# Optimization experiments

Hardware: AMD Instinct MI355X
Metric: run time of the kernel (lower is better)

The kernel has to match this reference:

```python
import jax, jax.numpy as jnp
import numpy as np

H = 768      # hidden_size
NH = 12      # num_attention_heads
DH = H // NH # attention_head_size
FF = 3072    # intermediate_size
E = 4        # n_expert
B, S = 8, 512
EPS = 1e-12


def _layernorm(x, g, b):
    mu = jnp.mean(x, axis=-1, keepdims=True)
    var = jnp.var(x, axis=-1, keepdims=True)
    return (x - mu) * jax.lax.rsqrt(var + EPS) * g + b


def _expert_linear(x, W, b, expert_idx):
    # W: [E, in, out], b: [E, out]; gather per-sample expert weights, then batched GEMM.
    # Mathematically identical to running every expert then slicing (single_select_fwd).
    Wg = W[expert_idx]            # [B, in, out]
    bg = b[expert_idx]            # [B, out]
    return jnp.einsum('bsi,bio->bso', x, Wg) + bg[:, None, :]


def setup_inputs() -> dict:
    key = jax.random.key(0)
    ks = jax.random.split(key, 16)
    sc = 0.02
    inp = {
        'hidden_states': jax.random.normal(ks[0], (B, S, H), jnp.float32),
        'expert_idx': jax.random.randint(ks[1], (B,), 0, E, jnp.int64) if jax.config.read('jax_enable_x64') else jax.random.randint(ks[1], (B,), 0, E).astype(jnp.int32),
        'attention_mask': jnp.zeros((B, 1, 1, S), jnp.float32),
        'Wq': sc * jax.random.normal(ks[2], (E, H, H), jnp.float32),
        'bq': jnp.zeros((E, H), jnp.float32),
        'Wk': sc * jax.random.normal(ks[3], (E, H, H), jnp.float32),
        'bk': jnp.zeros((E, H), jnp.float32),
        'Wv': sc * jax.random.normal(ks[4], (E, H, H), jnp.float32),
        'bv': jnp.zeros((E, H), jnp.float32),
        'Wo': sc * jax.random.normal(ks[5], (E, H, H), jnp.float32),
        'bo': jnp.zeros((E, H), jnp.float32),
        'ln1_g': jnp.ones((H,), jnp.float32),
        'ln1_b': jnp.zeros((H,), jnp.float32),
        'Wi': sc * jax.random.normal(ks[6], (E, H, FF), jnp.float32),
        'bi': jnp.zeros((E, FF), jnp.float32),
        'Wout': sc * jax.random.normal(ks[7], (E, FF, H), jnp.float32),
        'bout': jnp.zeros((E, H), jnp.float32),
        'ln2_g': jnp.ones((H,), jnp.float32),
        'ln2_b': jnp.zeros((H,), jnp.float32),
    }
    return inp


def reference(hidden_states, expert_idx, attention_mask, Wq, bq, Wk, bk, Wv, bv,
              Wo, bo, ln1_g, ln1_b, Wi, bi, Wout, bout, ln2_g, ln2_b):
    b, s, h = hidden_states.shape
    # --- MoE self-attention (per-sample expert QKV) ---
    q = _expert_linear(hidden_states, Wq, bq, expert_idx).reshape(b, s, NH, DH).transpose(0, 2, 1, 3)
    k = _expert_linear(hidden_states, Wk, bk, expert_idx).reshape(b, s, NH, DH).transpose(0, 2, 1, 3)
    v = _expert_linear(hidden_states, Wv, bv, expert_idx).reshape(b, s, NH, DH).transpose(0, 2, 1, 3)
    scores = jnp.einsum('bhqd,bhkd->bhqk', q, k) / np.sqrt(DH).astype(np.float32)
    scores = scores + attention_mask
    probs = jax.nn.softmax(scores, axis=-1)
    ctx = jnp.einsum('bhqk,bhkd->bhqd', probs, v).transpose(0, 2, 1, 3).reshape(b, s, h)
    # --- MoE self-output: dense + residual + LN ---
    attn_out = _expert_linear(ctx, Wo, bo, expert_idx)
    x = _layernorm(attn_out + hidden_states, ln1_g, ln1_b)
    # --- MoE FFN: intermediate (GELU) + output + residual + LN ---
    hmid = jax.nn.gelu(_expert_linear(x, Wi, bi, expert_idx), approximate=False)
    ffn = _expert_linear(hmid, Wout, bout, expert_idx)
    return _layernorm(ffn + x, ln2_g, ln2_b)
```

## Files before the change

kernel.cpp:

```cpp
#include <hip/hip_runtime.h>
#include <cstdint>
#include <cstddef>

constexpr int CB  = 8;
constexpr int CS  = 512;
constexpr int CH  = 768;
constexpr int CNH = 12;
constexpr int CDH = 64;
constexpr int CFF = 3072;
constexpr int CE  = 4;
constexpr int C3H = 3 * CH;

using f32x4  = __attribute__((ext_vector_type(4))) float;
using bf16x8 = __attribute__((ext_vector_type(8))) short;

__device__ __forceinline__ short f2bf(float x) {
  union { float f; uint32_t u; } v; v.f = x;
  return (short)((v.u + 0x7fffu + ((v.u >> 16) & 1u)) >> 16);
}

__device__ __forceinline__ void gload_lds16(const void* g, void* l) {
  __builtin_amdgcn_global_load_lds((const __attribute__((address_space(1))) void*)g,
                                   (__attribute__((address_space(3))) void*)l,
                                   16, 0, 0);
}

#define VMCNT(n)  asm volatile("s_waitcnt vmcnt(" #n ")" ::: "memory")

__global__ void cvt_bf16_kernel(const float* __restrict__ in, short* __restrict__ out, int n4) {
  int i = blockIdx.x * blockDim.x + threadIdx.x;
  if (i < n4) {
    float4 v = ((const float4*)in)[i];
    short4 o;
    o.x = f2bf(v.x); o.y = f2bf(v.y); o.z = f2bf(v.z); o.w = f2bf(v.w);
    ((short4*)out)[i] = o;
  }
}

__device__ __forceinline__ bool expert_used(const int* __restrict__ eidx, int e) {
  bool u = false;
#pragma unroll
  for (int s = 0; s < CB; ++s) u |= (eidx[s] == e);
  return u;
}

__device__ __forceinline__ void tpose_body(const float* __restrict__ Wb,
                                           short* __restrict__ Wtb, int K, int N) {
  __shared__ __align__(16) short Ts[64 * 68];
  const int n0 = blockIdx.x * 64, k0 = blockIdx.y * 64;
  const int t  = threadIdx.x;
  const int tn = t & 15, tk = t >> 4;
#pragma unroll
  for (int p = 0; p < 4; ++p) {
    int k = k0 + p * 16 + tk;
    float4 v = *(const float4*)(Wb + (size_t)k * N + n0 + tn * 4);
#pragma unroll
    for (int j = 0; j < 4; ++j)
      Ts[(tn * 4 + j) * 68 + p * 16 + tk] = f2bf(((const float*)&v)[j]);
  }
  __syncthreads();
#pragma unroll
  for (int p = 0; p < 4; ++p) {
    int n = n0 + p * 16 + tk;
    uint2 o = *(const uint2*)(Ts + (p * 16 + tk) * 68 + tn * 4);
    *(uint2*)(Wtb + (size_t)n * K + k0 + tn * 4) = o;
  }
}

__global__ void tpose_cvt_kernel(const float* __restrict__ W, short* __restrict__ Wt,
                                 const int* __restrict__ eidx, int K, int N) {
  const int e = blockIdx.z;
  if (!expert_used(eidx, e)) return;
  tpose_body(W + (size_t)e * K * N, Wt + (size_t)e * K * N, K, N);
}

__global__ void tpose4_kernel(const float* __restrict__ Wq, const float* __restrict__ Wk,
                              const float* __restrict__ Wv, const float* __restrict__ Wo,
                              const int* __restrict__ eidx,
                              short* __restrict__ Wqkvt, short* __restrict__ Wot) {
  const int z = blockIdx.z, e = z >> 2, m = z & 3;
  if (!expert_used(eidx, e)) return;
  const float* W = (m == 0) ? Wq : (m == 1) ? Wk : (m == 2) ? Wv : Wo;
  const float* Wb = W + (size_t)e * CH * CH;
  short* dst = (m == 3) ? (Wot + (size_t)e * CH * CH)
                        : (Wqkvt + ((size_t)e * C3H + m * CH) * CH);
  tpose_body(Wb, dst, CH, CH);
}

__global__ void qkv_bias_kernel(const float* __restrict__ bq, const float* __restrict__ bk,
                                const float* __restrict__ bv, float* __restrict__ dst) {
  int i = blockIdx.x * 256 + threadIdx.x;
  if (i >= CE * C3H) return;
  int e = i / C3H, r = i % C3H;
  int m = r / CH, c = r % CH;
  const float* s = (m == 0) ? bq : (m == 1) ? bk : bv;
  dst[i] = s[e * CH + c];
}

template <int BM, int BN, int TPB, int K, int NTN, int KSPLIT, int ACT, bool OB16>
__global__ __launch_bounds__(TPB, (TPB == 512 ? 2 : 3))
void gemm3_kernel(const short* __restrict__ A, const short* __restrict__ Wt,
                  const float* __restrict__ bias, const int* __restrict__ eidx,
                  char* __restrict__ out,
                  size_t wtExpStride, int biasStride, int outLd, size_t outKsStride) {
  constexpr int WAVES = TPB / 64;
  constexpr int WARPS_N = BN / 64, WARPS_M = WAVES / WARPS_N;
  constexpr int WM = BM / WARPS_M, MI = WM / 16;
  constexpr int NT = K / KSPLIT / 32;
  constexpr int JC = 4096 / BM;
  constexpr int MTS = CS / BM;
  __shared__ __align__(16) short As[2][BM * 32];
  __shared__ __align__(16) short Bs[2][BN * 32];
  const int t = threadIdx.x, w = t >> 6, l = t & 63, lr = l & 15, lg = l >> 4;

  int exv[CB];
#pragma unroll
  for (int s = 0; s < CB; ++s) exv[s] = eidx[s];
  uint32_t epack = 0;
#pragma unroll
  for (int s = 0; s < CB; ++s) epack |= (uint32_t)exv[s] << (2 * s);
  int c0 = 0, c1 = 0, c2 = 0, c3 = 0;
#pragma unroll
  for (int s = 0; s < CB; ++s) {
    c0 += (exv[s] == 0); c1 += (exv[s] == 1); c2 += (exv[s] == 2); c3 += (exv[s] == 3);
  }
  int p0 = 0, p1 = c0, p2 = c0 + c1, p3 = c0 + c1 + c2;
  uint32_t sortedPack = 0;
#pragma unroll
  for (int s = 0; s < CB; ++s) {
    int e = exv[s];
    int p = (e == 0) ? p0 : (e == 1) ? p1 : (e == 2) ? p2 : p3;
    sortedPack |= (uint32_t)s << (4 * p);
    p0 += (e == 0); p1 += (e == 1); p2 += (e == 2); p3 += (e == 3);
  }
  const int chunk = (int)gridDim.x >> 3;
  const int W_ = ((int)blockIdx.x & 7) * chunk + ((int)blockIdx.x >> 3);
  const int ks = W_ / (JC * NTN);
  const int r1 = W_ - ks * (JC * NTN);
  const int j  = r1 / NTN, nt = r1 - j * NTN;
  const int sample = (int)((sortedPack >> (4 * (j / MTS))) & 7);
  const int jj = j % MTS;
  const int e  = (int)((epack >> (2 * sample)) & 3);
  const int mrow0 = sample * CS + jj * BM;
  const int kBase = ks * NT * 32;

  const int srow = t >> 2;
  const int gcol = (((t & 3) ^ ((t >> 3) & 3)) * 8);
  const short* aSrc = A + (size_t)(mrow0 + srow) * K + kBase + gcol;
  const short* bSrc = Wt + (size_t)e * wtExpStride + (size_t)(nt * BN + srow) * K + kBase + gcol;
  constexpr int ROWS_PER_ISS = TPB / 4;
  const size_t issStride = (size_t)ROWS_PER_ISS * K;

  const int wrow = (w / WARPS_N) * WM, wn = (w % WARPS_N) * 64;
  const int rswz = (lg ^ ((lr >> 1) & 3)) * 8;
  int aoff[MI], boff[4];
#pragma unroll
  for (int mi = 0; mi < MI; ++mi) aoff[mi] = (wrow + mi * 16 + lr) * 32 + rswz;
#pragma unroll
  for (int ni = 0; ni < 4; ++ni)  boff[ni] = (wn + ni * 16 + lr) * 32 + rswz;

  f32x4 acc[MI][4] = {};

  auto STAGE = [&](int buf, int kt) {
    const short* as = aSrc + kt * 32;
#pragma unroll
    for (int i = 0; i < BM / ROWS_PER_ISS; ++i)
      gload_lds16(as + i * issStride, &As[buf][i * TPB * 8 + t * 8]);
    const short* bs = bSrc + kt * 32;
#pragma unroll
    for (int i = 0; i < BN / ROWS_PER_ISS; ++i)
      gload_lds16(bs + i * issStride, &Bs[buf][i * TPB * 8 + t * 8]);
  };

  STAGE(0, 0);
  VMCNT(0);
  __builtin_amdgcn_s_barrier();
  __builtin_amdgcn_sched_barrier(0);

  for (int kt = 0; kt < NT; ++kt) {
    const int buf = kt & 1;
    if (kt + 1 < NT) STAGE(buf ^ 1, kt + 1);
    bf16x8 bfr[4], af[MI];
#pragma unroll
    for (int ni = 0; ni < 4; ++ni)  bfr[ni] = *(const bf16x8*)(&Bs[buf][boff[ni]]);
#pragma unroll
    for (int mi = 0; mi < MI; ++mi) af[mi] = *(const bf16x8*)(&As[buf][aoff[mi]]);
    __builtin_amdgcn_s_setprio(1);
#pragma unroll
    for (int mi = 0; mi < MI; ++mi)
#pragma unroll
      for (int ni = 0; ni < 4; ++ni)
        acc[mi][ni] = __builtin_amdgcn_mfma_f32_16x16x32_bf16(af[mi], bfr[ni], acc[mi][ni], 0, 0, 0);
    __builtin_amdgcn_s_setprio(0);
    VMCNT(0);
    __builtin_amdgcn_s_barrier();
    __builtin_amdgcn_sched_barrier(0);
  }

  float* outF = (float*)out + (size_t)ks * outKsStride;
#pragma unroll
  for (int ni = 0; ni < 4; ++ni) {
    const int col = nt * BN + wn + ni * 16 + lr;
    const float bv = bias ? bias[e * biasStride + col] : 0.0f;
#pragma unroll
    for (int mi = 0; mi < MI; ++mi) {
      const int row0 = mrow0 + wrow + mi * 16 + lg * 4;
#pragma unroll
      for (int r = 0; r < 4; ++r) {
        float v = acc[mi][ni][r] + bv;
        if (ACT == 1) v = 0.5f * v * (1.0f + erff(v * 0.70710678118654752f));
        if (OB16) ((short*)out)[(size_t)(row0 + r) * outLd + col] = f2bf(v);
        else      outF[(size_t)(row0 + r) * outLd + col] = v;
      }
    }
  }
}

__global__ void attn_kernel(const short* __restrict__ QKV, const float* __restrict__ mask,
                            short* __restrict__ ctx) {
  __shared__ __align__(16) short Vt[2][64 * 40];
  __shared__ __align__(16) short Pt[4][2][16 * 40];
  const int bh = blockIdx.x;
  const int b = bh / CNH, h = bh % CNH;
  const int qt = blockIdx.y;
  const int t = threadIdx.x, w = t >> 6, l = t & 63, lr = l & 15, lg = l >> 4;

  const size_t bS = (size_t)b * CS;
  const short* Qh = QKV + bS * C3H + h * CDH;
  const short* Kh = Qh + CH;
  const short* Vh = Qh + 2 * CH;
  const float* mrow = mask + bS;

  const int qrow = qt * 64 + w * 16 + lr;
  bf16x8 qa[2];
  qa[0] = *(const bf16x8*)(Qh + (size_t)qrow * C3H + lg * 8);
  qa[1] = *(const bf16x8*)(Qh + (size_t)qrow * C3H + 32 + lg * 8);

  f32x4 o[4] = {};
  float lp[4] = {0.f, 0.f, 0.f, 0.f};

  const int dh = t & 63, kg = t >> 6;
  {
    short v8[8];
#pragma unroll
    for (int j = 0; j < 8; ++j) v8[j] = Vh[(size_t)(kg * 8 + j) * C3H + dh];
    uint32_t p0 = (uint32_t)(uint16_t)v8[0] | ((uint32_t)(uint16_t)v8[1] << 16);
    uint32_t p1 = (uint32_t)(uint16_t)v8[2] | ((uint32_t)(uint16_t)v8[3] << 16);
    uint32_t p2 = (uint32_t)(uint16_t)v8[4] | ((uint32_t)(uint16_t)v8[5] << 16);
    uint32_t p3 = (uint32_t)(uint16_t)v8[6] | ((uint32_t)(uint16_t)v8[7] << 16);
    uint4 pk = {p0, p1, p2, p3};
    *(uint4*)(&Vt[0][dh * 40 + kg * 8]) = pk;
  }

  for (int tt = 0; tt < CS / 32; ++tt) {
    const int k0 = tt * 32;
    __syncthreads();

    f32x4 sacc[2] = {};
#pragma unroll
    for (int n = 0; n < 2; ++n) {
      bf16x8 kb0 = *(const bf16x8*)(Kh + (size_t)(k0 + n * 16 + lr) * C3H + lg * 8);
      bf16x8 kb1 = *(const bf16x8*)(Kh + (size_t)(k0 + n * 16 + lr) * C3H + 32 + lg * 8);
      sacc[n] = __builtin_amdgcn_mfma_f32_16x16x32_bf16(qa[0], kb0, sacc[n], 0, 0, 0);
      sacc[n] = __builtin_amdgcn_mfma_f32_16x16x32_bf16(qa[1], kb1, sacc[n], 0, 0, 0);
    }

    if (tt + 1 < CS / 32) {
      const int k1 = k0 + 32;
      short v8[8];
#pragma unroll
      for (int j = 0; j < 8; ++j) v8[j] = Vh[(size_t)(k1 + kg * 8 + j) * C3H + dh];
      uint32_t p0 = (uint32_t)(uint16_t)v8[0] | ((uint32_t)(uint16_t)v8[1] << 16);
      uint32_t p1 = (uint32_t)(uint16_t)v8[2] | ((uint32_t)(uint16_t)v8[3] << 16);
      uint32_t p2 = (uint32_t)(uint16_t)v8[4] | ((uint32_t)(uint16_t)v8[5] << 16);
      uint32_t p3 = (uint32_t)(uint16_t)v8[6] | ((uint32_t)(uint16_t)v8[7] << 16);
      uint4 pk = {p0, p1, p2, p3};
      *(uint4*)(&Vt[(tt + 1) & 1][dh * 40 + kg * 8]) = pk;
    }

    const int pb = tt & 1;
#pragma unroll
    for (int n = 0; n < 2; ++n) {
      float mv = mrow[k0 + n * 16 + lr];
#pragma unroll
      for (int r = 0; r < 4; ++r) {
        float s = sacc[n][r] * 0.125f + mv;
        float e = __expf(s);
        lp[r] += e;
        Pt[w][pb][(lg * 4 + r) * 40 + n * 16 + lr] = f2bf(e);
      }
    }

    bf16x8 pa = *(const bf16x8*)(&Pt[w][pb][lr * 40 + lg * 8]);
#pragma unroll
    for (int d = 0; d < 4; ++d) {
      bf16x8 vbf = *(const bf16x8*)(&Vt[tt & 1][(d * 16 + lr) * 40 + lg * 8]);
      o[d] = __builtin_amdgcn_mfma_f32_16x16x32_bf16(pa, vbf, o[d], 0, 0, 0);
    }
  }

#pragma unroll
  for (int r = 0; r < 4; ++r) {
    float s = lp[r];
    s += __shfl_xor(s, 1); s += __shfl_xor(s, 2);
    s += __shfl_xor(s, 4); s += __shfl_xor(s, 8);
    lp[r] = 1.0f / s;
  }
#pragma unroll
  for (int d = 0; d < 4; ++d)
#pragma unroll
    for (int r = 0; r < 4; ++r) {
      int row = qt * 64 + w * 16 + lg * 4 + r;
      ctx[(bS + row) * CH + h * CDH + d * 16 + lr] = f2bf(o[d][r] * lp[r]);
    }
}

__global__ void ln_kernel(const float* __restrict__ xin, const float* __restrict__ res,
                          const float* __restrict__ g, const float* __restrict__ bta,
                          float* __restrict__ out32, short* __restrict__ out16) {
  const int row = blockIdx.x;
  const int l = threadIdx.x;
  const float* xr = xin + (size_t)row * CH;
  const float* rr = res + (size_t)row * CH;
  float4 v[3];
  float sum = 0.f, ss = 0.f;
#pragma unroll
  for (int j = 0; j < 3; ++j) {
    float4 a = *(const float4*)(xr + j * 256 + l * 4);
    float4 b = *(const float4*)(rr + j * 256 + l * 4);
    a.x += b.x; a.y += b.y; a.z += b.z; a.w += b.w;
    v[j] = a;
    sum += a.x + a.y + a.z + a.w;
    ss  += a.x * a.x + a.y * a.y + a.z * a.z + a.w * a.w;
  }
#pragma unroll
  for (int m = 1; m < 64; m <<= 1) { sum += __shfl_xor(sum, m); ss += __shfl_xor(ss, m); }
  const float mean = sum * (1.0f / CH);
  const float var  = ss * (1.0f / CH) - mean * mean;
  const float rstd = rsqrtf(var + 1e-12f);
#pragma unroll
  for (int j = 0; j < 3; ++j) {
    float4 gg = *(const float4*)(g   + j * 256 + l * 4);
    float4 bb = *(const float4*)(bta + j * 256 + l * 4);
    float4 a = v[j], y;
    y.x = (a.x - mean) * rstd * gg.x + bb.x;
    y.y = (a.y - mean) * rstd * gg.y + bb.y;
    y.z = (a.z - mean) * rstd * gg.z + bb.z;
    y.w = (a.w - mean) * rstd * gg.w + bb.w;
    *(float4*)(out32 + (size_t)row * CH + j * 256 + l * 4) = y;
    if (out16) {
      short4 o;
      o.x = f2bf(y.x); o.y = f2bf(y.y); o.z = f2bf(y.z); o.w = f2bf(y.w);
      *(short4*)(out16 + (size_t)row * CH + j * 256 + l * 4) = o;
    }
  }
}

__global__ void ln2_kernel(const float* __restrict__ p0, const float* __restrict__ p1,
                           const float* __restrict__ res,
                           const float* __restrict__ bout, const int* __restrict__ eidx,
                           const float* __restrict__ g, const float* __restrict__ bta,
                           float* __restrict__ out) {
  const int row = blockIdx.x;
  const int l = threadIdx.x;
  const int e = eidx[row >> 9];
  const float* xr0 = p0 + (size_t)row * CH;
  const float* xr1 = p1 + (size_t)row * CH;
  const float* rr  = res + (size_t)row * CH;
  const float* bo  = bout + (size_t)e * CH;
  float4 v[3];
  float sum = 0.f, ss = 0.f;
#pragma unroll
  for (int j = 0; j < 3; ++j) {
    float4 a = *(const float4*)(xr0 + j * 256 + l * 4);
    float4 c = *(const float4*)(xr1 + j * 256 + l * 4);
    float4 b = *(const float4*)(rr + j * 256 + l * 4);
    float4 bb = *(const float4*)(bo + j * 256 + l * 4);
    a.x += c.x + b.x + bb.x; a.y += c.y + b.y + bb.y;
    a.z += c.z + b.z + bb.z; a.w += c.w + b.w + bb.w;
    v[j] = a;
    sum += a.x + a.y + a.z + a.w;
    ss  += a.x * a.x + a.y * a.y + a.z * a.z + a.w * a.w;
  }
#pragma unroll
  for (int m = 1; m < 64; m <<= 1) { sum += __shfl_xor(sum, m); ss += __shfl_xor(ss, m); }
  const float mean = sum * (1.0f / CH);
  const float var  = ss * (1.0f / CH) - mean * mean;
  const float rstd = rsqrtf(var + 1e-12f);
#pragma unroll
  for (int j = 0; j < 3; ++j) {
    float4 gg = *(const float4*)(g   + j * 256 + l * 4);
    float4 bb = *(const float4*)(bta + j * 256 + l * 4);
    float4 a = v[j], y;
    y.x = (a.x - mean) * rstd * gg.x + bb.x;
    y.y = (a.y - mean) * rstd * gg.y + bb.y;
    y.z = (a.z - mean) * rstd * gg.z + bb.z;
    y.w = (a.w - mean) * rstd * gg.w + bb.w;
    *(float4*)(out + (size_t)row * CH + j * 256 + l * 4) = y;
  }
}

extern "C" void kernel_launch(void* const* d_in, const int* in_sizes, int n_in,
                              void* d_out, int out_size, void* d_ws, size_t ws_size,
                              hipStream_t stream) {
  (void)in_sizes; (void)n_in; (void)out_size; (void)ws_size;
  const float* hidden = (const float*)d_in[0];
  const int*   eidx   = (const int*)d_in[1];
  const float* mask   = (const float*)d_in[2];
  const float* Wq   = (const float*)d_in[3];
  const float* bq   = (const float*)d_in[4];
  const float* Wk   = (const float*)d_in[5];
  const float* bk   = (const float*)d_in[6];
  const float* Wv   = (const float*)d_in[7];
  const float* bv   = (const float*)d_in[8];
  const float* Wo   = (const float*)d_in[9];
  const float* bo   = (const float*)d_in[10];
  const float* ln1g = (const float*)d_in[11];
  const float* ln1b = (const float*)d_in[12];
  const float* Wi   = (const float*)d_in[13];
  const float* bi   = (const float*)d_in[14];
  const float* Wout = (const float*)d_in[15];
  const float* bout = (const float*)d_in[16];
  const float* ln2g = (const float*)d_in[17];
  const float* ln2b = (const float*)d_in[18];

  char* ws = (char*)d_ws;
  size_t off = 0;
  auto alloc = [&](size_t bytes) {
    void* p = ws + off;
    off += (bytes + 255) & ~(size_t)255;
    return p;
  };
  const size_t M = (size_t)CB * CS;
  short* Xb    = (short*)alloc(M * CH * 2);
  char*  Rbig  = (char*)alloc(M * CFF * 2);
  char*  Rcx   = (char*)alloc(M * CH * 4);
  float* ffnp  = (float*)alloc(2 * M * CH * 4);
  float* qkvbias = (float*)alloc(CE * C3H * 4);
  short* Wqkvt = (short*)alloc((size_t)CE * C3H * CH * 2);
  short* Wot   = (short*)alloc((size_t)CE * CH * CH * 2);
  short* Wit   = (short*)alloc((size_t)CE * CH * CFF * 2);
  short* Wo2t  = (short*)alloc((size_t)CE * CFF * CH * 2);
  short* QKVb     = (short*)Rbig;
  short* hmid     = (short*)Rbig;
  short* ctxb     = (short*)Rcx;
  float* x1       = (float*)Rcx;
  short* x1b      = Xb;
  float* attn_out = (float*)Wqkvt;

  const int n4 = (int)(M * CH / 4);
  cvt_bf16_kernel<<<(n4 + 255) / 256, 256, 0, stream>>>(hidden, Xb, n4);
  tpose4_kernel<<<dim3(CH / 64, CH / 64, 4 * CE), 256, 0, stream>>>(Wq, Wk, Wv, Wo, eidx, Wqkvt, Wot);
  tpose_cvt_kernel<<<dim3(CFF / 64, CH / 64, CE), 256, 0, stream>>>(Wi, Wit, eidx, CH, CFF);
  tpose_cvt_kernel<<<dim3(CH / 64, CFF / 64, CE), 256, 0, stream>>>(Wout, Wo2t, eidx, CFF, CH);
  qkv_bias_kernel<<<(CE * C3H + 255) / 256, 256, 0, stream>>>(bq, bk, bv, qkvbias);

  gemm3_kernel<256, 256, 512, CH, 9, 1, 0, true><<<144, 512, 0, stream>>>(
      Xb, Wqkvt, qkvbias, eidx, (char*)QKVb, (size_t)C3H * CH, C3H, C3H, 0);
  attn_kernel<<<dim3(CB * CNH, CS / 64), 256, 0, stream>>>(QKVb, mask, ctxb);
  gemm3_kernel<128, 128, 256, CH, 6, 1, 0, false><<<192, 256, 0, stream>>>(
      ctxb, Wot, bo, eidx, (char*)attn_out, (size_t)CH * CH, CH, CH, 0);
  ln_kernel<<<(int)M, 64, 0, stream>>>(attn_out, hidden, ln1g, ln1b, x1, x1b);
  gemm3_kernel<256, 256, 512, CH, 12, 1, 1, true><<<192, 512, 0, stream>>>(
      x1b, Wit, bi, eidx, (char*)hmid, (size_t)CH * CFF, CFF, CFF, 0);
  gemm3_kernel<128, 128, 256, CFF, 6, 2, 0, false><<<384, 256, 0, stream>>>(
      hmid, Wo2t, nullptr, eidx, (char*)ffnp, (size_t)CFF * CH, CH, CH, M * CH);
  ln2_kernel<<<(int)M, 64, 0, stream>>>(ffnp, ffnp + M * CH, x1, bout, eidx,
                                        ln2g, ln2b, (float*)d_out);
}
```

Before: 220.4 us.

## Double GEMM K-tile to 64 with 8-slot XOR swizzle and relaxed vmcnt wait

The expert GEMM kernel now stages 64-wide K slices instead of 32, using an 8-slot XOR swizzle for LDS rows and two MFMA sub-steps per tile. This halves the number of K iterations and barriers. The wait is restructured so the next stage's loads are issued before waiting, with vmcnt(8) waiting only on the current buffer. The aim is better overlap of global-to-LDS traffic with MFMA work. The cost is doubled LDS use: the 256x256 config now needs 128KB, which may allow only one block per CU, so occupancy drops.

```diff
diff --git a/kernel.cpp b/kernel.cpp
--- a/kernel.cpp
+++ b/kernel.cpp
@@ -26,6 +26,7 @@
 }
 
 #define VMCNT(n)  asm volatile("s_waitcnt vmcnt(" #n ")" ::: "memory")
+#define SCHEDB()  __builtin_amdgcn_sched_barrier(0)
 
 __global__ void cvt_bf16_kernel(const float* __restrict__ in, short* __restrict__ out, int n4) {
   int i = blockIdx.x * blockDim.x + threadIdx.x;
@@ -98,19 +99,19 @@
 }
 
 template <int BM, int BN, int TPB, int K, int NTN, int KSPLIT, int ACT, bool OB16>
-__global__ __launch_bounds__(TPB, (TPB == 512 ? 2 : 3))
-void gemm3_kernel(const short* __restrict__ A, const short* __restrict__ Wt,
+__global__ __launch_bounds__(TPB, 2)
+void gemm4_kernel(const short* __restrict__ A, const short* __restrict__ Wt,
                   const float* __restrict__ bias, const int* __restrict__ eidx,
                   char* __restrict__ out,
                   size_t wtExpStride, int biasStride, int outLd, size_t outKsStride) {
   constexpr int WAVES = TPB / 64;
   constexpr int WARPS_N = BN / 64, WARPS_M = WAVES / WARPS_N;
   constexpr int WM = BM / WARPS_M, MI = WM / 16;
-  constexpr int NT = K / KSPLIT / 32;
+  constexpr int NT = K / KSPLIT / 64;
   constexpr int JC = 4096 / BM;
   constexpr int MTS = CS / BM;
-  __shared__ __align__(16) short As[2][BM * 32];
-  __shared__ __align__(16) short Bs[2][BN * 32];
+  __shared__ __align__(16) short As[2][BM * 64];
+  __shared__ __align__(16) short Bs[2][BN * 64];
   const int t = threadIdx.x, w = t >> 6, l = t & 63, lr = l & 15, lg = l >> 4;
 
   int exv[CB];
@@ -119,10 +120,10 @@
   uint32_t epack = 0;
 #pragma unroll
   for (int s = 0; s < CB; ++s) epack |= (uint32_t)exv[s] << (2 * s);
-  int c0 = 0, c1 = 0, c2 = 0, c3 = 0;
+  int c0 = 0, c1 = 0, c2 = 0;
 #pragma unroll
   for (int s = 0; s < CB; ++s) {
-    c0 += (exv[s] == 0); c1 += (exv[s] == 1); c2 += (exv[s] == 2); c3 += (exv[s] == 3);
+    c0 += (exv[s] == 0); c1 += (exv[s] == 1); c2 += (exv[s] == 2);
   }
   int p0 = 0, p1 = c0, p2 = c0 + c1, p3 = c0 + c1 + c2;
   uint32_t sortedPack = 0;
@@ -142,59 +143,68 @@
   const int jj = j % MTS;
   const int e  = (int)((epack >> (2 * sample)) & 3);
   const int mrow0 = sample * CS + jj * BM;
-  const int kBase = ks * NT * 32;
-
-  const int srow = t >> 2;
-  const int gcol = (((t & 3) ^ ((t >> 3) & 3)) * 8);
+  const int kBase = ks * NT * 64;
+
+  const int srow = t >> 3;
+  const int gcol = (((t & 7) ^ ((t >> 3) & 7)) * 8);
   const short* aSrc = A + (size_t)(mrow0 + srow) * K + kBase + gcol;
   const short* bSrc = Wt + (size_t)e * wtExpStride + (size_t)(nt * BN + srow) * K + kBase + gcol;
-  constexpr int ROWS_PER_ISS = TPB / 4;
-  const size_t issStride = (size_t)ROWS_PER_ISS * K;
+  constexpr int RPI = TPB / 8;
+  const size_t issStride = (size_t)RPI * K;
 
   const int wrow = (w / WARPS_N) * WM, wn = (w % WARPS_N) * 64;
-  const int rswz = (lg ^ ((lr >> 1) & 3)) * 8;
-  int aoff[MI], boff[4];
-#pragma unroll
-  for (int mi = 0; mi < MI; ++mi) aoff[mi] = (wrow + mi * 16 + lr) * 32 + rswz;
-#pragma unroll
-  for (int ni = 0; ni < 4; ++ni)  boff[ni] = (wn + ni * 16 + lr) * 32 + rswz;
+  int aoff[2][MI], boff[2][4];
+#pragma unroll
+  for (int kk = 0; kk < 2; ++kk) {
+    const int slot = (kk * 4 + lg) ^ (lr & 7);
+#pragma unroll
+    for (int mi = 0; mi < MI; ++mi)
+      aoff[kk][mi] = (wrow + mi * 16 + lr) * 64 + slot * 8;
+#pragma unroll
+    for (int ni = 0; ni < 4; ++ni)
+      boff[kk][ni] = (wn + ni * 16 + lr) * 64 + slot * 8;
+  }
 
   f32x4 acc[MI][4] = {};
 
   auto STAGE = [&](int buf, int kt) {
-    const short* as = aSrc + kt * 32;
-#pragma unroll
-    for (int i = 0; i < BM / ROWS_PER_ISS; ++i)
+    const short* as = aSrc + (size_t)kt * 64;
+#pragma unroll
+    for (int i = 0; i < BM / RPI; ++i)
       gload_lds16(as + i * issStride, &As[buf][i * TPB * 8 + t * 8]);
-    const short* bs = bSrc + kt * 32;
-#pragma unroll
-    for (int i = 0; i < BN / ROWS_PER_ISS; ++i)
+    const short* bs = bSrc + (size_t)kt * 64;
+#pragma unroll
+    for (int i = 0; i < BN / RPI; ++i)
       gload_lds16(bs + i * issStride, &Bs[buf][i * TPB * 8 + t * 8]);
   };
 
   STAGE(0, 0);
-  VMCNT(0);
-  __builtin_amdgcn_s_barrier();
-  __builtin_amdgcn_sched_barrier(0);
-
   for (int kt = 0; kt < NT; ++kt) {
     const int buf = kt & 1;
-    if (kt + 1 < NT) STAGE(buf ^ 1, kt + 1);
-    bf16x8 bfr[4], af[MI];
-#pragma unroll
-    for (int ni = 0; ni < 4; ++ni)  bfr[ni] = *(const bf16x8*)(&Bs[buf][boff[ni]]);
-#pragma unroll
-    for (int mi = 0; mi < MI; ++mi) af[mi] = *(const bf16x8*)(&As[buf][aoff[mi]]);
+    if (kt + 1 < NT) { STAGE(buf ^ 1, kt + 1); VMCNT(8); }
+    else             { VMCNT(0); }
+    __builtin_amdgcn_s_barrier();
+    SCHEDB();
+    bf16x8 af[2][MI], bfr[2][4];
+#pragma unroll
+    for (int kk = 0; kk < 2; ++kk) {
+#pragma unroll
+      for (int ni = 0; ni < 4; ++ni) bfr[kk][ni] = *(const bf16x8*)(&Bs[buf][boff[kk][ni]]);
+#pragma unroll
+      for (int mi = 0; mi < MI; ++mi) af[kk][mi] = *(const bf16x8*)(&As[buf][aoff[kk][mi]]);
+    }
     __builtin_amdgcn_s_setprio(1);
 #pragma unroll
-    for (int mi = 0; mi < MI; ++mi)
-#pragma unroll
-      for (int ni = 0; ni < 4; ++ni)
-        acc[mi][ni] = __builtin_amdgcn_mfma_f32_16x16x32_bf16(af[mi], bfr[ni], acc[mi][ni], 0, 0, 0);
+    for (int kk = 0; kk < 2; ++kk)
+#pragma unroll
+      for (int mi = 0; mi < MI; ++mi)
+#pragma unroll
+        for (int ni = 0; ni < 4; ++ni)
+          acc[mi][ni] = __builtin_amdgcn_mfma_f32_16x16x32_bf16(af[kk][mi], bfr[kk][ni],
+                                                                acc[mi][ni], 0, 0, 0);
     __builtin_amdgcn_s_setprio(0);
-    VMCNT(0);
     __builtin_amdgcn_s_barrier();
-    __builtin_amdgcn_sched_barrier(0);
+    SCHEDB();
   }
 
   float* outF = (float*)out + (size_t)ks * outKsStride;
@@ -455,15 +465,15 @@
   tpose_cvt_kernel<<<dim3(CH / 64, CFF / 64, CE), 256, 0, stream>>>(Wout, Wo2t, eidx, CFF, CH);
   qkv_bias_kernel<<<(CE * C3H + 255) / 256, 256, 0, stream>>>(bq, bk, bv, qkvbias);
 
-  gemm3_kernel<256, 256, 512, CH, 9, 1, 0, true><<<144, 512, 0, stream>>>(
+  gemm4_kernel<256, 256, 512, CH, 9, 1, 0, true><<<144, 512, 0, stream>>>(
       Xb, Wqkvt, qkvbias, eidx, (char*)QKVb, (size_t)C3H * CH, C3H, C3H, 0);
   attn_kernel<<<dim3(CB * CNH, CS / 64), 256, 0, stream>>>(QKVb, mask, ctxb);
-  gemm3_kernel<128, 128, 256, CH, 6, 1, 0, false><<<192, 256, 0, stream>>>(
+  gemm4_kernel<128, 128, 256, CH, 6, 1, 0, false><<<192, 256, 0, stream>>>(
       ctxb, Wot, bo, eidx, (char*)attn_out, (size_t)CH * CH, CH, CH, 0);
   ln_kernel<<<(int)M, 64, 0, stream>>>(attn_out, hidden, ln1g, ln1b, x1, x1b);
-  gemm3_kernel<256, 256, 512, CH, 12, 1, 1, true><<<192, 512, 0, stream>>>(
+  gemm4_kernel<256, 256, 512, CH, 12, 1, 1, true><<<192, 512, 0, stream>>>(
       x1b, Wit, bi, eidx, (char*)hmid, (size_t)CH * CFF, CFF, CFF, 0);
-  gemm3_kernel<128, 128, 256, CFF, 6, 2, 0, false><<<384, 256, 0, stream>>>(
+  gemm4_kernel<128, 128, 256, CFF, 6, 2, 0, false><<<384, 256, 0, stream>>>(
       hmid, Wo2t, nullptr, eidx, (char*)ffnp, (size_t)CFF * CH, CH, CH, M * CH);
   ln2_kernel<<<(int)M, 64, 0, stream>>>(ffnp, ffnp + M * CH, x1, bout, eidx,
                                         ln2g, ln2b, (float*)d_out);
```

New measurement: 201.4 us. 8.6% less time.
